# Kernel optimization log

Measured on AMD Instinct MI355X. Metric: run time of the kernel, lower is better.

Reference implementation:

```python
import jax, jax.numpy as jnp
import numpy as np

N, N_IN, N_OUT, D, IN_DIM, OUT_DIM = 512, 64, 16, 256, 64, 64

def _xavier(k, shape, fan_in, fan_out):
    lim = float(np.sqrt(6.0 / (fan_in + fan_out)))
    return jax.random.uniform(k, shape, minval=-lim, maxval=lim, dtype=jnp.float32)

def _lin_w(k, fo, fi):
    lim = float(np.sqrt(1.0 / fi))
    return jax.random.uniform(k, (fo, fi), minval=-lim, maxval=lim, dtype=jnp.float32)

def setup_inputs() -> dict:
    ks = jax.random.split(jax.random.key(0), 16)
    return {
        "x": jax.random.normal(ks[0], (N, N_IN, D), dtype=jnp.float32),
        "mask": jnp.ones((N, N_IN), dtype=jnp.float32),
        "Wcap": _xavier(ks[1], (N_IN, D, IN_DIM), D, IN_DIM),
        "Bcap": jnp.zeros((N_IN, IN_DIM), jnp.float32),
        "Wvotes": _xavier(ks[2], (N_IN, N_OUT, IN_DIM, OUT_DIM), IN_DIM, OUT_DIM),
        "Bvotes": jnp.zeros((N_IN, N_OUT, 1, OUT_DIM), jnp.float32),
        "score_W": _lin_w(ks[3], 1, OUT_DIM), "score_b": jnp.zeros((1,), jnp.float32),
        "alpha_W": _lin_w(ks[4], 1, OUT_DIM), "alpha_b": jnp.zeros((1,), jnp.float32),
        "fe1_W": _lin_w(ks[5], OUT_DIM, OUT_DIM), "fe1_b": jnp.zeros((OUT_DIM,), jnp.float32),
        "fe2_W": _lin_w(ks[6], OUT_DIM, OUT_DIM), "fe2_b": jnp.zeros((OUT_DIM,), jnp.float32),
        "fn1_W": _lin_w(ks[7], OUT_DIM, OUT_DIM), "fn1_b": jnp.zeros((OUT_DIM,), jnp.float32),
        "fn2_W": _lin_w(ks[8], OUT_DIM, OUT_DIM), "fn2_b": jnp.zeros((OUT_DIM,), jnp.float32),
        "iters": 3,
    }

def _gelu(x):
    return jax.nn.gelu(x, approximate=False)  # torch F.gelu default (erf)

def _lin(x, W, b):
    return x @ W.T + b  # torch nn.Linear convention: W is (out, in)

def reference(x, mask, Wcap, Bcap, Wvotes, Bvotes, score_W, score_b,
              alpha_W, alpha_b, fe1_W, fe1_b, fe2_W, fe2_b,
              fn1_W, fn1_b, fn2_W, fn2_b, iters):
    # attention mask: -inf where padded, 0 elsewhere; shape (N, n_in, 1, 1)
    att = jnp.where(mask == 0.0, -jnp.inf, 0.0).astype(x.dtype)[:, :, None, None]
    # per-input-capsule projection: (N, n_in, D) x (n_in, D, in_dim) -> (N, n_in, in_dim)
    xc = _gelu(jnp.einsum('nid,idh->nih', x, Wcap) + Bcap)
    # votes: (N, n_in, n_out, out_dim)
    votes = jnp.einsum('nid,ijdh->nijh', xc, Wvotes) + Bvotes[:, :, 0, :]
    m = mask[:, :, None, None]
    votes = votes * m
    fn_v = _lin(votes, fn1_W, fn1_b)  # (N, n_in, n_out, out_dim)
    fe_v = _lin(votes, fe1_W, fe1_b)
    bij = _lin(votes, score_W, score_b)  # (N, n_in, n_out, 1)
    aij = jax.nn.softmax(bij * m + att, axis=1)
    vj = None
    for i in range(iters):
        if i != 0:
            new_vj = _gelu(jnp.sum(aij * votes, axis=1))  # (N, n_out, out_dim)
            alpha = jax.nn.sigmoid(_lin(new_vj, alpha_W, alpha_b))
            vj = alpha * new_vj + (1.0 - alpha) * vj
        else:
            vj = _gelu(jnp.sum(aij * votes, axis=1))
        if i != iters - 1:
            vj_ = vj[:, None]  # (N, 1, n_out, out_dim)
            E = jnp.sum(fe_v * _lin(vj_, fe2_W, fe2_b), axis=-1, keepdims=True)
            M = -jnp.sum(jnp.abs(fn_v - _lin(vj_, fn2_W, fn2_b)), axis=-1, keepdims=True)
            aij = jnp.tanh(E) * jax.nn.sigmoid(M * m + att)
    return vj  # (N, n_out, out_dim)
```

## Files before the change

kernel.cpp:

```cpp
#include <hip/hip_runtime.h>
#include <hip/hip_bf16.h>

#define NN 512
#define NI 64
#define NJ 16
#define DD 256
#define HI 64
#define HO 64

typedef unsigned int  u32;
typedef unsigned short u16;

typedef _Float16 f16;
typedef __attribute__((ext_vector_type(2))) _Float16 f16x2;
typedef __attribute__((ext_vector_type(8))) _Float16 f16x8;
typedef __attribute__((ext_vector_type(4))) float f32x4;

__device__ __forceinline__ float gelu_exact(float x){
    return 0.5f * x * (1.0f + erff(x * 0.7071067811865476f));
}
__device__ __forceinline__ float sigm(float x){
    return 1.0f / (1.0f + __expf(-x));
}
__device__ __forceinline__ u16 f2h(float f){
    union { f16 h; u16 u; } c; c.h = (f16)f; return c.u;
}
__device__ __forceinline__ float h2f(u16 u){
    union { u16 u; f16 h; } c; c.u = u; return (float)c.h;
}
__device__ __forceinline__ f16x2 bch2(u32 x){
    union { u32 u; f16x2 h; } c; c.u = x; return c.h;
}
__device__ __forceinline__ f16x2 habs2(f16x2 a){
    union { f16x2 h; u32 u; } c; c.h = a; c.u &= 0x7FFF7FFFu; return c.h;
}
__device__ __forceinline__ float dot2f(u32 a, u32 b, float acc){
    return __builtin_amdgcn_fdot2(bch2(a), bch2(b), acc, false);
}
__device__ __forceinline__ float dot8h(uint4 q, uint4 v, float acc){
    acc = dot2f(q.x, v.x, acc);
    acc = dot2f(q.y, v.y, acc);
    acc = dot2f(q.z, v.z, acc);
    acc = dot2f(q.w, v.w, acc);
    return acc;
}
__device__ __forceinline__ float bcast_lane(float v, int lane){
    return __uint_as_float(__builtin_amdgcn_readlane(__float_as_uint(v), lane));
}

__global__ __launch_bounds__(256) void k_prep_small(
    const float* __restrict__ fn1W, const float* __restrict__ fe2W,
    const float* __restrict__ fn2W, const float* __restrict__ fe1W,
    u16* __restrict__ fn1wf, u16* __restrict__ wAh2,
    u16* __restrict__ wBh2, u16* __restrict__ wCth2)
{
    const int t = threadIdx.x;
    #pragma unroll
    for (int u = 0; u < 16; ++u){
        const int o = t + u * 256;
        {
            const int c = o >> 9, row = (o >> 3) & 63, e = o & 7;
            wAh2[o]  = f2h(fe2W[row * 64 + c * 8 + e]);
            wBh2[o]  = f2h(fn2W[row * 64 + c * 8 + e]);
            wCth2[o] = f2h(fe1W[(c * 8 + e) * 64 + row]);
        }
        {
            const int q = o >> 9, ll = (o >> 3) & 63, e = o & 7;
            const int ht = q >> 1, hf = q & 1, lr = ll & 15, lg = ll >> 4;
            fn1wf[o] = f2h(fn1W[(ht * 16 + lr) * 64 + hf * 32 + lg * 8 + e]);
        }
    }
}

__global__ __launch_bounds__(256) void k_xc(const float* __restrict__ x,
    const float* __restrict__ Wcap, const float* __restrict__ Bcap,
    u16* __restrict__ xcb)
{
    __shared__ u16 wt_l[16384];
    __shared__ u16 strip[4][1024];
    const int nc = blockIdx.x, i = blockIdx.y;
    const int n0 = nc * 64;
    const int t = threadIdx.x;
    const int w = t >> 6, l = t & 63;
    const int lr = l & 15, lg = l >> 4;

    {
        const float* wsrc = Wcap + (size_t)i * (DD * HI);
        const int h = t & 63, kg = t >> 6;
        #pragma unroll
        for (int p = 0; p < 32; ++p){
            const int k = (p * 4 + kg) * 2;
            u32 lo = f2h(wsrc[(size_t)k * HI + h]);
            u32 hi = f2h(wsrc[(size_t)(k + 1) * HI + h]);
            const int g = k >> 3;
            *(u32*)&wt_l[h * 256 + ((g ^ (h & 7)) << 3) + (k & 7)] = lo | (hi << 16);
        }
    }
    __syncthreads();

    const float* xrow = x + ((size_t)(n0 + 16 * w + lr) * NI + i) * DD;
    f32x4 acc[4] = {};
    #pragma unroll
    for (int ks = 0; ks < 8; ++ks){
        float4 f0 = *(const float4*)(xrow + ks * 32 + lg * 8);
        float4 f1 = *(const float4*)(xrow + ks * 32 + lg * 8 + 4);
        f16x8 a;
        a[0] = (f16)f0.x; a[1] = (f16)f0.y; a[2] = (f16)f0.z; a[3] = (f16)f0.w;
        a[4] = (f16)f1.x; a[5] = (f16)f1.y; a[6] = (f16)f1.z; a[7] = (f16)f1.w;
        #pragma unroll
        for (int ht = 0; ht < 4; ++ht){
            const int h = ht * 16 + lr;
            f16x8 b = *(const f16x8*)&wt_l[h * 256 + (((ks * 4 + lg) ^ (lr & 7)) << 3)];
            acc[ht] = __builtin_amdgcn_mfma_f32_16x16x32_f16(a, b, acc[ht], 0, 0, 0);
        }
    }

    u16* st = strip[w];
    #pragma unroll
    for (int ht = 0; ht < 4; ++ht){
        const int h = ht * 16 + lr, g = h >> 3;
        const float bc = Bcap[i * HI + h];
        #pragma unroll
        for (int r = 0; r < 4; ++r){
            const int m = lg * 4 + r;
            st[m * 64 + ((g ^ (m & 7)) << 3) + (h & 7)] = f2h(gelu_exact(acc[ht][r] + bc));
        }
    }
    {
        const int row = l >> 2, g0 = (l & 3) * 2;
        const size_t off = ((size_t)(n0 + 16 * w + row) * NI + i) * HI;
        #pragma unroll
        for (int gg = g0; gg < g0 + 2; ++gg){
            uint4 q = *(const uint4*)&st[row * 64 + ((gg ^ (row & 7)) << 3)];
            *(uint4*)(xcb + off + gg * 8) = q;
        }
    }
}

__global__ __launch_bounds__(256) void k_votes(
    const u16* __restrict__ xcb, const float* __restrict__ Wv,
    const float* __restrict__ Bv, const float* __restrict__ mask,
    const float* __restrict__ scoreW, const float* __restrict__ scoreb,
    u16* __restrict__ votes, float* __restrict__ bij)
{
    __shared__ u16 vstrip[4][1024];
    const int i = blockIdx.x, j = blockIdx.y;
    const int t = threadIdx.x, w = t >> 6, l = t & 63;
    const int lr = l & 15, lg = l >> 4;
    const int isw = i & 7;

    f16x8 wb0[4], wb1[4];
    const float* wvp = Wv + (size_t)(i * NJ + j) * 4096;
    float bv[4], swv[4];
    #pragma unroll
    for (int ht = 0; ht < 4; ++ht){
        const int h = ht * 16 + lr;
        #pragma unroll
        for (int e = 0; e < 8; ++e){
            wb0[ht][e] = (f16)wvp[(lg * 8 + e) * 64 + h];
            wb1[ht][e] = (f16)wvp[(32 + lg * 8 + e) * 64 + h];
        }
        bv[ht]  = Bv[(size_t)(i * NJ + j) * HO + h];
        swv[ht] = scoreW[h];
    }
    const float sb = scoreb[0];
    u16* vst = vstrip[w];

    for (int nc = 0; nc < 8; ++nc){
        const int n0 = nc * 64 + 16 * w;
        const u16* ar = xcb + ((size_t)(n0 + lr) * NI + i) * HI + lg * 8;
        f16x8 a0 = *(const f16x8*)ar;
        f16x8 a1 = *(const f16x8*)(ar + 32);
        float mk[4];
        #pragma unroll
        for (int r = 0; r < 4; ++r)
            mk[r] = mask[(size_t)(n0 + lg * 4 + r) * NI + i];

        float p[4] = {};
        #pragma unroll
        for (int ht = 0; ht < 4; ++ht){
            f32x4 c4 = {};
            c4 = __builtin_amdgcn_mfma_f32_16x16x32_f16(a0, wb0[ht], c4, 0, 0, 0);
            c4 = __builtin_amdgcn_mfma_f32_16x16x32_f16(a1, wb1[ht], c4, 0, 0, 0);
            const int h = ht * 16 + lr, gp = h >> 3;
            #pragma unroll
            for (int r = 0; r < 4; ++r){
                const int rs = lg * 4 + r;
                float val = (c4[r] + bv[ht]) * mk[r];
                p[r] += val * swv[ht];
                vst[rs * 64 + ((gp ^ (rs & 7)) << 3) + (h & 7)] = f2h(val);
            }
        }
        #pragma unroll
        for (int r = 0; r < 4; ++r){
            float s = p[r];
            s += __shfl_xor(s, 1); s += __shfl_xor(s, 2);
            s += __shfl_xor(s, 4); s += __shfl_xor(s, 8);
            if (lr == 0)
                bij[((size_t)(n0 + lg * 4 + r) * NJ + j) * NI + i] = s + sb;
        }

        {
            const int row = l >> 2, g0 = (l & 3) * 2;
            const size_t off = (((size_t)(nc * 64 + 16 * w + row) * NJ + j) * NI + i) * HO;
            #pragma unroll
            for (int gg = g0; gg < g0 + 2; ++gg){
                uint4 qv = *(const uint4*)&vst[row * 64 + ((gg ^ (row & 7)) << 3)];
                *(uint4*)(votes + off + ((gg ^ isw) << 3)) = qv;
            }
        }
    }
}

__global__ __launch_bounds__(256) void k_route(
    const u16* __restrict__ votes, const float* __restrict__ bijg,
    const float* __restrict__ mask,
    const float* __restrict__ alphaW, const float* __restrict__ alphab,
    const u16* __restrict__ wAh2, const float* __restrict__ fe2b,
    const u16* __restrict__ wBh2, const float* __restrict__ fn2b,
    const u16* __restrict__ wCth2, const float* __restrict__ fe1b,
    const u16* __restrict__ fn1wf, const float* __restrict__ fn1b,
    const int* __restrict__ itersp, float* __restrict__ out)
{
    __shared__ u16 t_l[4][4096];
    __shared__ float s_M[4][64];
    __shared__ alignas(16) u16 s_vjh[4][64];
    __shared__ alignas(16) u16 s_gh[4][64];
    __shared__ alignas(16) u16 s_wh[4][64];
    __shared__ alignas(16) u16 s_uh[4][64];

    const int t = threadIdx.x;
    const int wid = t >> 6;
    const int l = t & 63;
    const int lr = l & 15, lg = l >> 4;
    const int pair = blockIdx.x * 4 + wid;
    const int n = pair >> 4, j = pair & 15;
    const size_t base = ((size_t)n * NJ + j) * (size_t)(NI * HO);

    u16*   tile = t_l[wid];
    float* Mw   = s_M[wid];
    u16*   vjh  = s_vjh[wid];
    u16*   sgh  = s_gh[wid];
    u16*   swh  = s_wh[wid];
    u16*   suh  = s_uh[wid];

    {
        const uint4* src = (const uint4*)(votes + base);
        #pragma unroll
        for (int half = 0; half < 2; ++half){
            uint4 tb[4];
            #pragma unroll
            for (int c = 0; c < 4; ++c) tb[c] = src[(half * 4 + c) * 64 + l];
            #pragma unroll
            for (int c = 0; c < 4; ++c)
                *(uint4*)&tile[((half * 4 + c) * 64 + l) * 8] = tb[c];
        }
    }

    const float mki  = mask[(size_t)n * NI + l];
    const float atti = (mki == 0.f) ? -3.0e38f : 0.f;

    float aijr;
    {
        float s = bijg[((size_t)n * NJ + j) * NI + l] * mki + atti;
        float mx = s;
        #pragma unroll
        for (int off = 32; off; off >>= 1) mx = fmaxf(mx, __shfl_xor(mx, off));
        float pe = __expf(s - mx);
        float sm = pe;
        #pragma unroll
        for (int off = 32; off; off >>= 1) sm += __shfl_xor(sm, off);
        aijr = pe / sm;
    }

    uint2 fnvh[4][4];
    #pragma unroll
    for (int itile = 0; itile < 4; ++itile){
        const int row = itile * 16 + lr;
        const int key = row & 7;
        const u16* vr = tile + row * 64;
        f16x8 vb0 = *(const f16x8*)&vr[(lg ^ key) << 3];
        f16x8 vb1 = *(const f16x8*)&vr[((lg + 4) ^ key) << 3];
        #pragma unroll
        for (int ht = 0; ht < 4; ++ht){
            f16x8 a0 = *(const f16x8*)&fn1wf[(ht * 2 + 0) * 512 + l * 8];
            f16x8 a1 = *(const f16x8*)&fn1wf[(ht * 2 + 1) * 512 + l * 8];
            f32x4 c4 = {};
            c4 = __builtin_amdgcn_mfma_f32_16x16x32_f16(a0, vb0, c4, 0, 0, 0);
            c4 = __builtin_amdgcn_mfma_f32_16x16x32_f16(a1, vb1, c4, 0, 0, 0);
            const int h0 = ht * 16 + lg * 4;
            u32 lo = (u32)f2h(c4[0] + fn1b[h0])     | ((u32)f2h(c4[1] + fn1b[h0 + 1]) << 16);
            u32 hi = (u32)f2h(c4[2] + fn1b[h0 + 2]) | ((u32)f2h(c4[3] + fn1b[h0 + 3]) << 16);
            fnvh[itile][ht] = make_uint2(lo, hi);
        }
    }

    const int iters = itersp[0];
    float vj = 0.f;
    for (int it = 0; it < iters; ++it){
        const int gsh = (l >> 3) << 3;
        const int lo7 = l & 7;
        float ac0 = 0.f, ac1 = 0.f, ac2 = 0.f, ac3 = 0.f;
        #pragma unroll
        for (int ii = 0; ii < 16; ++ii){
            const int sw = (gsh ^ ((ii & 7) << 3)) + lo7;
            ac0 += bcast_lane(aijr, ii)      * h2f(tile[ ii       * 64 + sw]);
            ac1 += bcast_lane(aijr, ii + 16) * h2f(tile[(ii + 16) * 64 + sw]);
            ac2 += bcast_lane(aijr, ii + 32) * h2f(tile[(ii + 32) * 64 + sw]);
            ac3 += bcast_lane(aijr, ii + 48) * h2f(tile[(ii + 48) * 64 + sw]);
        }
        float nv = gelu_exact((ac0 + ac1) + (ac2 + ac3));
        if (it == 0) vj = nv;
        else {
            float dv = nv * alphaW[l];
            #pragma unroll
            for (int off = 32; off; off >>= 1) dv += __shfl_xor(dv, off);
            float alpha = sigm(dv + alphab[0]);
            vj = alpha * nv + (1.f - alpha) * vj;
        }
        if (it == iters - 1) break;
        vjh[l] = f2h(vj);

        float ga = 0.f, wacc = 0.f;
        #pragma unroll 1
        for (int c2 = 0; c2 < 4; ++c2){
            uint4 vq0 = *(const uint4*)&vjh[(2 * c2) * 8];
            uint4 vq1 = *(const uint4*)&vjh[(2 * c2 + 1) * 8];
            uint4 wa0 = *(const uint4*)&wAh2[((2 * c2) * 64 + l) * 8];
            uint4 wa1 = *(const uint4*)&wAh2[((2 * c2 + 1) * 64 + l) * 8];
            uint4 wb0 = *(const uint4*)&wBh2[((2 * c2) * 64 + l) * 8];
            uint4 wb1 = *(const uint4*)&wBh2[((2 * c2 + 1) * 64 + l) * 8];
            ga   = dot8h(wa0, vq0, ga);
            ga   = dot8h(wa1, vq1, ga);
            wacc = dot8h(wb0, vq0, wacc);
            wacc = dot8h(wb1, vq1, wacc);
        }
        float g = ga + fe2b[l];
        sgh[l] = f2h(g);
        swh[l] = f2h(wacc + fn2b[l]);

        float ua = 0.f;
        #pragma unroll 1
        for (int c2 = 0; c2 < 4; ++c2){
            uint4 gq0 = *(const uint4*)&sgh[(2 * c2) * 8];
            uint4 gq1 = *(const uint4*)&sgh[(2 * c2 + 1) * 8];
            uint4 wc0 = *(const uint4*)&wCth2[((2 * c2) * 64 + l) * 8];
            uint4 wc1 = *(const uint4*)&wCth2[((2 * c2 + 1) * 64 + l) * 8];
            ua = dot8h(wc0, gq0, ua);
            ua = dot8h(wc1, gq1, ua);
        }
        suh[l] = f2h(ua);
        float cv = fe1b[l] * g;
        #pragma unroll
        for (int off = 32; off; off >>= 1) cv += __shfl_xor(cv, off);

        uint2 wq[4];
        #pragma unroll
        for (int ht = 0; ht < 4; ++ht)
            wq[ht] = *(const uint2*)&swh[ht * 16 + lg * 4];
        #pragma unroll
        for (int itile = 0; itile < 4; ++itile){
            f16x2 macc = {(f16)0.f, (f16)0.f};
            #pragma unroll
            for (int ht = 0; ht < 4; ++ht){
                macc += habs2(bch2(fnvh[itile][ht].x) - bch2(wq[ht].x));
                macc += habs2(bch2(fnvh[itile][ht].y) - bch2(wq[ht].y));
            }
            float m = (float)macc[0] + (float)macc[1];
            m += __shfl_xor(m, 16);
            m += __shfl_xor(m, 32);
            if (l < 16) Mw[itile * 16 + l] = -m;
        }

        float e = cv;
        #pragma unroll 1
        for (int c2 = 0; c2 < 4; ++c2){
            uint4 q0 = *(const uint4*)&tile[l * 64 + (((2 * c2)     ^ (l & 7)) << 3)];
            uint4 q1 = *(const uint4*)&tile[l * 64 + (((2 * c2 + 1) ^ (l & 7)) << 3)];
            e = dot8h(q0, *(const uint4*)&suh[(2 * c2) * 8], e);
            e = dot8h(q1, *(const uint4*)&suh[(2 * c2 + 1) * 8], e);
        }
        aijr = tanhf(e) * sigm(Mw[l] * mki + atti);
    }

    out[((size_t)n * NJ + j) * HO + l] = vj;
}

extern "C" void kernel_launch(void* const* d_in, const int* in_sizes, int n_in,
                              void* d_out, int out_size, void* d_ws, size_t ws_size,
                              hipStream_t stream)
{
    (void)in_sizes; (void)n_in; (void)out_size; (void)ws_size;
    const float* x      = (const float*)d_in[0];
    const float* mask   = (const float*)d_in[1];
    const float* Wcap   = (const float*)d_in[2];
    const float* Bcap   = (const float*)d_in[3];
    const float* Wv     = (const float*)d_in[4];
    const float* Bv     = (const float*)d_in[5];
    const float* scoreW = (const float*)d_in[6];
    const float* scoreb = (const float*)d_in[7];
    const float* alphaW = (const float*)d_in[8];
    const float* alphab = (const float*)d_in[9];
    const float* fe1W   = (const float*)d_in[10];
    const float* fe1b   = (const float*)d_in[11];
    const float* fe2W   = (const float*)d_in[12];
    const float* fe2b   = (const float*)d_in[13];
    const float* fn1W   = (const float*)d_in[14];
    const float* fn1b   = (const float*)d_in[15];
    const float* fn2W   = (const float*)d_in[16];
    const float* fn2b   = (const float*)d_in[17];
    const int*   itersp = (const int*)d_in[18];
    float* out = (float*)d_out;

    char* ws = (char*)d_ws;
    u16*   xcb   = (u16*)ws;
    u16*   vts   = (u16*)(ws + 4194304);
    float* bij   = (float*)(ws + 71303168);
    u16*   fn1wf = (u16*)(ws + 73400320);
    u16*   wAh2  = (u16*)(ws + 73408512);
    u16*   wBh2  = (u16*)(ws + 73416704);
    u16*   wCth2 = (u16*)(ws + 73424896);

    k_prep_small<<<1, 256, 0, stream>>>(fn1W, fe2W, fn2W, fe1W,
                                        fn1wf, wAh2, wBh2, wCth2);
    k_xc        <<<dim3(8, 64), 256, 0, stream>>>(x, Wcap, Bcap, xcb);
    k_votes     <<<dim3(64, 16), 256, 0, stream>>>(xcb, Wv, Bv, mask,
                                                   scoreW, scoreb, vts, bij);
    k_route     <<<2048, 256, 0, stream>>>(vts, bij, mask, alphaW, alphab,
                                           wAh2, fe2b, wBh2, fn2b, wCth2, fe1b,
                                           fn1wf, fn1b, itersp, out);
}
```

Before: 89.49 us.

## Load route tiles directly to LDS, remap xc blocks, parallelize weight prep

The route kernel now streams its votes tile from global memory straight into LDS with global_load_lds, instead of staging it through registers. The softmax then runs while those loads are in flight, and a waitcnt is placed before the MFMA stage. The xc kernel uses a flattened 1D grid with a remapped block index so that blocks sharing the same Wcap slice are spread across the XCDs. The small weight-prep kernel now runs on 16 blocks instead of looping inside a single block. The direct-to-LDS path relies on the linear per-lane destination layout matching the original tile indexing. It also depends on hardware ordering for the wait.

```diff
diff --git a/kernel.cpp b/kernel.cpp
--- a/kernel.cpp
+++ b/kernel.cpp
@@ -16,6 +16,9 @@
 typedef __attribute__((ext_vector_type(8))) _Float16 f16x8;
 typedef __attribute__((ext_vector_type(4))) float f32x4;
 
+typedef __attribute__((address_space(3))) void  lds_void;
+typedef const __attribute__((address_space(1))) void glob_void;
+
 __device__ __forceinline__ float gelu_exact(float x){
     return 0.5f * x * (1.0f + erff(x * 0.7071067811865476f));
 }
@@ -54,21 +57,17 @@
     u16* __restrict__ fn1wf, u16* __restrict__ wAh2,
     u16* __restrict__ wBh2, u16* __restrict__ wCth2)
 {
-    const int t = threadIdx.x;
-    #pragma unroll
-    for (int u = 0; u < 16; ++u){
-        const int o = t + u * 256;
-        {
-            const int c = o >> 9, row = (o >> 3) & 63, e = o & 7;
-            wAh2[o]  = f2h(fe2W[row * 64 + c * 8 + e]);
-            wBh2[o]  = f2h(fn2W[row * 64 + c * 8 + e]);
-            wCth2[o] = f2h(fe1W[(c * 8 + e) * 64 + row]);
-        }
-        {
-            const int q = o >> 9, ll = (o >> 3) & 63, e = o & 7;
-            const int ht = q >> 1, hf = q & 1, lr = ll & 15, lg = ll >> 4;
-            fn1wf[o] = f2h(fn1W[(ht * 16 + lr) * 64 + hf * 32 + lg * 8 + e]);
-        }
+    const int o = threadIdx.x + blockIdx.x * 256;
+    {
+        const int c = o >> 9, row = (o >> 3) & 63, e = o & 7;
+        wAh2[o]  = f2h(fe2W[row * 64 + c * 8 + e]);
+        wBh2[o]  = f2h(fn2W[row * 64 + c * 8 + e]);
+        wCth2[o] = f2h(fe1W[(c * 8 + e) * 64 + row]);
+    }
+    {
+        const int q = o >> 9, ll = (o >> 3) & 63, e = o & 7;
+        const int ht = q >> 1, hf = q & 1, lr = ll & 15, lg = ll >> 4;
+        fn1wf[o] = f2h(fn1W[(ht * 16 + lr) * 64 + hf * 32 + lg * 8 + e]);
     }
 }
 
@@ -78,7 +77,9 @@
 {
     __shared__ u16 wt_l[16384];
     __shared__ u16 strip[4][1024];
-    const int nc = blockIdx.x, i = blockIdx.y;
+    const int id = blockIdx.x;
+    const int i  = ((id & 7) << 3) | (id >> 6);
+    const int nc = (id >> 3) & 7;
     const int n0 = nc * 64;
     const int t = threadIdx.x;
     const int w = t >> 6, l = t & 63;
@@ -245,15 +246,13 @@
     u16*   suh  = s_uh[wid];
 
     {
-        const uint4* src = (const uint4*)(votes + base);
-        #pragma unroll
-        for (int half = 0; half < 2; ++half){
-            uint4 tb[4];
-            #pragma unroll
-            for (int c = 0; c < 4; ++c) tb[c] = src[(half * 4 + c) * 64 + l];
-            #pragma unroll
-            for (int c = 0; c < 4; ++c)
-                *(uint4*)&tile[((half * 4 + c) * 64 + l) * 8] = tb[c];
+        const uint4* srcq = (const uint4*)(votes + base);
+        #pragma unroll
+        for (int c = 0; c < 8; ++c){
+            __builtin_amdgcn_global_load_lds(
+                (glob_void*)(srcq + c * 64 + l),
+                (lds_void*)(tile + c * 512),
+                16, 0, 0);
         }
     }
 
@@ -272,6 +271,9 @@
         for (int off = 32; off; off >>= 1) sm += __shfl_xor(sm, off);
         aijr = pe / sm;
     }
+
+    asm volatile("s_waitcnt vmcnt(0)" ::: "memory");
+    __builtin_amdgcn_sched_barrier(0);
 
     uint2 fnvh[4][4];
     #pragma unroll
@@ -421,9 +423,9 @@
     u16*   wBh2  = (u16*)(ws + 73416704);
     u16*   wCth2 = (u16*)(ws + 73424896);
 
-    k_prep_small<<<1, 256, 0, stream>>>(fn1W, fe2W, fn2W, fe1W,
-                                        fn1wf, wAh2, wBh2, wCth2);
-    k_xc        <<<dim3(8, 64), 256, 0, stream>>>(x, Wcap, Bcap, xcb);
+    k_prep_small<<<16, 256, 0, stream>>>(fn1W, fe2W, fn2W, fe1W,
+                                         fn1wf, wAh2, wBh2, wCth2);
+    k_xc        <<<512, 256, 0, stream>>>(x, Wcap, Bcap, xcb);
     k_votes     <<<dim3(64, 16), 256, 0, stream>>>(xcb, Wv, Bv, mask,
                                                    scoreW, scoreb, vts, bij);
     k_route     <<<2048, 256, 0, stream>>>(vts, bij, mask, alphaW, alphab,
```

New measurement: 88.85 us. About the same (-0.7%).
